# Kernel tuning notes

Measured on AMD Instinct MI355X. Metric: run time of the kernel, lower is better.

## Reference

```python
import jax, jax.numpy as jnp
import numpy as np

B = 65536
IN_DIM = 512
H0, H1 = 256, 128
HEAD_H = 64
D = 12
K_MAX = 3
EPS = 1e-5
# predecessor indices per disease (topologically ordered DAG)
PRED_LISTS = [[], [0], [0], [1, 2], [0, 3], [2], [4, 5], [1, 6], [3, 7], [6, 8], [5, 9], [8, 10, 9]]


def setup_inputs() -> dict:
    key = jax.random.key(0)
    ks = jax.random.split(key, 16)
    x = jax.random.normal(ks[0], (B, IN_DIM), jnp.float32)
    enc_W0 = jax.random.normal(ks[1], (IN_DIM, H0), jnp.float32) * 0.04
    enc_b0 = jnp.zeros((H0,), jnp.float32)
    bn0_g = jnp.ones((H0,), jnp.float32)
    bn0_b = jnp.zeros((H0,), jnp.float32)
    bn0_m = jax.random.normal(ks[2], (H0,), jnp.float32) * 0.1
    bn0_v = jax.random.uniform(ks[3], (H0,), jnp.float32, 0.5, 1.5)
    enc_W1 = jax.random.normal(ks[4], (H0, H1), jnp.float32) * 0.06
    enc_b1 = jnp.zeros((H1,), jnp.float32)
    bn1_g = jnp.ones((H1,), jnp.float32)
    bn1_b = jnp.zeros((H1,), jnp.float32)
    bn1_m = jax.random.normal(ks[5], (H1,), jnp.float32) * 0.1
    bn1_v = jax.random.uniform(ks[6], (H1,), jnp.float32, 0.5, 1.5)
    w_init = jax.random.normal(ks[7], (D, H1), jnp.float32) * 0.09   # head.layer1 (pass-1 logit)
    b_init = jnp.zeros((D,), jnp.float32)
    Wz = jax.random.normal(ks[8], (D, H1, HEAD_H), jnp.float32) * 0.09   # head first layer, z-columns
    Wp = jax.random.normal(ks[9], (D, K_MAX, HEAD_H), jnp.float32) * 0.09  # head first layer, predecessor columns (padded)
    bh = jnp.zeros((D, HEAD_H), jnp.float32)
    Wo = jax.random.normal(ks[10], (D, HEAD_H), jnp.float32) * 0.12
    bo = jnp.zeros((D,), jnp.float32)
    idx = np.zeros((D, K_MAX), np.int32)
    w = np.zeros((D, K_MAX), np.float32)
    for d, preds in enumerate(PRED_LISTS):
        for j, p in enumerate(preds):
            idx[d, j] = p
            w[d, j] = 0.5  # DAG edge weight; zero entries are padding
    return {"x": x, "enc_W0": enc_W0, "enc_b0": enc_b0, "bn0_g": bn0_g, "bn0_b": bn0_b,
            "bn0_m": bn0_m, "bn0_v": bn0_v, "enc_W1": enc_W1, "enc_b1": enc_b1,
            "bn1_g": bn1_g, "bn1_b": bn1_b, "bn1_m": bn1_m, "bn1_v": bn1_v,
            "w_init": w_init, "b_init": b_init, "Wz": Wz, "Wp": Wp, "bh": bh,
            "Wo": Wo, "bo": bo, "pred_w": jnp.asarray(w), "pred_idx": jnp.asarray(idx)}


def reference(x, enc_W0, enc_b0, bn0_g, bn0_b, bn0_m, bn0_v, enc_W1, enc_b1,
              bn1_g, bn1_b, bn1_m, bn1_v, w_init, b_init, Wz, Wp, bh, Wo, bo,
              pred_w, pred_idx):
    # Shared encoder: Linear -> BatchNorm(eval stats) -> ReLU, twice (dropout identity at eval)
    h = x @ enc_W0 + enc_b0
    h = jax.nn.relu((h - bn0_m) * jax.lax.rsqrt(bn0_v + EPS) * bn0_g + bn0_b)
    z = h @ enc_W1 + enc_b1
    z = jax.nn.relu((z - bn1_m) * jax.lax.rsqrt(bn1_v + EPS) * bn1_g + bn1_b)  # [B, H1]
    # Pass 1: initial per-disease prediction = sigmoid(head.layer1(z))
    p = jax.nn.sigmoid(z @ w_init.T + b_init)  # [B, D]
    # Pass 2: DAG gather of predecessor predictions, edge-weighted; padding slots have weight 0
    aug = p[:, pred_idx] * pred_w  # [B, D, K_MAX]
    # Per-disease head: Linear(H1 + k -> HEAD_H) split into z-part + predecessor-part, ReLU, Linear(HEAD_H -> 1), sigmoid
    hid = jax.nn.relu(jnp.einsum('be,deh->bdh', z, Wz) + jnp.einsum('bdk,dkh->bdh', aug, Wp) + bh)
    out = jax.nn.sigmoid(jnp.einsum('bdh,dh->bd', hid, Wo) + bo)  # [B, D] = torch.cat of final_preds
    return out
```

## Files before the change

kernel.cpp:

```cpp
#include <hip/hip_runtime.h>
#include <stdint.h>

#define B_TOT   65536
#define IN_DIM  512
#define H0      256
#define H1      128
#define HH      64
#define NDIS    12

typedef __bf16 bf16_t;
typedef __bf16 bf16x4 __attribute__((ext_vector_type(4)));
typedef __bf16 bf16x8 __attribute__((ext_vector_type(8)));
typedef float  f32x4  __attribute__((ext_vector_type(4)));

#define WS_W0T   0u
#define WS_W1T   262144u
#define WS_WZT   327680u
#define WS_WIT   524288u
#define WS_AL0   528384u
#define WS_BE0   529408u
#define WS_AL1   530432u
#define WS_BE1   530944u
#define WS_NEED  531456u

#define L_PS     17408u
#define L_PART   22528u
#define L_TOTAL  34816u

__device__ __forceinline__ f32x4 MF(bf16x8 a, bf16x8 b, f32x4 c) {
    return __builtin_amdgcn_mfma_f32_16x16x32_bf16(a, b, c, 0, 0, 0);
}
__device__ __forceinline__ void BAR() {
    asm volatile("s_waitcnt lgkmcnt(0)\n\ts_barrier" ::: "memory");
}

#define PACK8(o, lo, hi) { o[0]=(bf16_t)lo[0]; o[1]=(bf16_t)lo[1]; o[2]=(bf16_t)lo[2]; o[3]=(bf16_t)lo[3]; \
                           o[4]=(bf16_t)hi[0]; o[5]=(bf16_t)hi[1]; o[6]=(bf16_t)hi[2]; o[7]=(bf16_t)hi[3]; }

__global__ void prep_kernel(const float* __restrict__ W0, const float* __restrict__ b0,
                            const float* __restrict__ g0, const float* __restrict__ bb0,
                            const float* __restrict__ mm0, const float* __restrict__ vv0,
                            const float* __restrict__ W1, const float* __restrict__ b1,
                            const float* __restrict__ g1, const float* __restrict__ bb1,
                            const float* __restrict__ mm1, const float* __restrict__ vv1,
                            const float* __restrict__ w_init, const float* __restrict__ Wz,
                            char* __restrict__ ws)
{
    bf16_t* W0t = (bf16_t*)(ws + WS_W0T);
    bf16_t* W1t = (bf16_t*)(ws + WS_W1T);
    bf16_t* Wzt = (bf16_t*)(ws + WS_WZT);
    bf16_t* wiT = (bf16_t*)(ws + WS_WIT);
    float* al0 = (float*)(ws + WS_AL0);
    float* be0 = (float*)(ws + WS_BE0);
    float* al1 = (float*)(ws + WS_AL1);
    float* be1 = (float*)(ws + WS_BE1);

    int t = blockIdx.x * 256 + threadIdx.x;

    {
        int c = t >> 9, k = t & 511;
        W0t[t] = (bf16_t)W0[k * H0 + c];
    }
    if (t < H1 * H0) {
        int c = t >> 8, k = t & 255;
        W1t[t] = (bf16_t)W1[k * H1 + c];
    }
    if (t < NDIS * HH * H1) {
        int d = t >> 13, r = t & 8191, h = r >> 7, e = r & 127;
        Wzt[t] = (bf16_t)Wz[d * 8192 + e * 64 + h];
    }
    if (t < 16 * H1) {
        int d = t >> 7, e = t & 127;
        wiT[t] = (d < NDIS) ? (bf16_t)w_init[d * H1 + e] : (bf16_t)0.0f;
    }
    if (t < H0) {
        float a = g0[t] * rsqrtf(vv0[t] + 1e-5f);
        al0[t] = a;
        be0[t] = (b0[t] - mm0[t]) * a + bb0[t];
    }
    if (t < H1) {
        float a = g1[t] * rsqrtf(vv1[t] + 1e-5f);
        al1[t] = a;
        be1[t] = (b1[t] - mm1[t]) * a + bb1[t];
    }
}

__global__ __launch_bounds__(256, 4) void fused_kernel(
    const float* __restrict__ x,
    const bf16_t* __restrict__ W0t, const bf16_t* __restrict__ W1t,
    const float* __restrict__ al0, const float* __restrict__ be0,
    const float* __restrict__ al1, const float* __restrict__ be1,
    const bf16_t* __restrict__ Wzt, const bf16_t* __restrict__ wiT,
    const float* __restrict__ b_init, const float* __restrict__ Wp,
    const float* __restrict__ bh, const float* __restrict__ Wo,
    const float* __restrict__ bo, const float* __restrict__ pred_w,
    const int* __restrict__ pred_idx, float* __restrict__ out)
{
    __shared__ __align__(16) char smem[L_TOTAL];

    const int tid  = threadIdx.x;
    const int lane = tid & 63, wid = tid >> 6;
    const int l15 = lane & 15, lg = lane >> 4;
    const int m0 = blockIdx.x * 64;

    bf16_t* xs = (bf16_t*)smem;

    const float *sgp0, *sgp1;
    int sd0, sd1;
    {
        int f0 = tid, f1 = tid + 256;
        int r0 = f0 >> 3, s0 = f0 & 7, r1 = f1 >> 3, s1 = f1 & 7;
        sgp0 = x + (size_t)(m0 + r0) * IN_DIM + s0 * 8;
        sgp1 = x + (size_t)(m0 + r1) * IN_DIM + s1 * 8;
        sd0 = r0 * 64 + ((s0 ^ (r0 & 7)) << 3);
        sd1 = r1 * 64 + ((s1 ^ (r1 & 7)) << 3);
    }
    const bf16_t* wg = W0t + (size_t)(wid * 64 + l15) * IN_DIM + lg * 8;
    const int xb0 = ((lg ^ (l15 & 7)) << 3);
    const int xb1 = (((4 | lg) ^ (l15 & 7)) << 3);
    const int xrow = l15 * 64;

    f32x4 acc[4][4] = {};
    f32x4 lo0, hi0, lo1, hi1;

    lo0 = *(const f32x4*)(sgp0);     hi0 = *(const f32x4*)(sgp0 + 4);
    lo1 = *(const f32x4*)(sgp1);     hi1 = *(const f32x4*)(sgp1 + 4);
    { bf16x8 o; PACK8(o, lo0, hi0); *(bf16x8*)(xs + sd0) = o; }
    { bf16x8 o; PACK8(o, lo1, hi1); *(bf16x8*)(xs + sd1) = o; }
    lo0 = *(const f32x4*)(sgp0 + 64); hi0 = *(const f32x4*)(sgp0 + 68);
    lo1 = *(const f32x4*)(sgp1 + 64); hi1 = *(const f32x4*)(sgp1 + 68);
    BAR();

    #pragma unroll 1
    for (int ks = 0; ks < 8; ++ks) {
        bf16x8 a0[4], a1[4];
        #pragma unroll
        for (int mf = 0; mf < 4; ++mf) {
            a0[mf] = *(const bf16x8*)(wg + mf * 16 * IN_DIM + ks * 64);
            a1[mf] = *(const bf16x8*)(wg + mf * 16 * IN_DIM + ks * 64 + 32);
        }
        if (ks < 7) {
            bf16_t* xw = xs + ((ks + 1) & 1) * 4096;
            { bf16x8 o; PACK8(o, lo0, hi0); *(bf16x8*)(xw + sd0) = o; }
            { bf16x8 o; PACK8(o, lo1, hi1); *(bf16x8*)(xw + sd1) = o; }
            if (ks < 6) {
                lo0 = *(const f32x4*)(sgp0 + (ks + 2) * 64); hi0 = *(const f32x4*)(sgp0 + (ks + 2) * 64 + 4);
                lo1 = *(const f32x4*)(sgp1 + (ks + 2) * 64); hi1 = *(const f32x4*)(sgp1 + (ks + 2) * 64 + 4);
            }
        }
        const bf16_t* xr = xs + (ks & 1) * 4096;
        #pragma unroll
        for (int nf = 0; nf < 4; ++nf) {
            bf16x8 b = *(const bf16x8*)(xr + nf * 1024 + xrow + xb0);
            #pragma unroll
            for (int mf = 0; mf < 4; ++mf) acc[mf][nf] = MF(a0[mf], b, acc[mf][nf]);
        }
        #pragma unroll
        for (int nf = 0; nf < 4; ++nf) {
            bf16x8 b = *(const bf16x8*)(xr + nf * 1024 + xrow + xb1);
            #pragma unroll
            for (int mf = 0; mf < 4; ++mf) acc[mf][nf] = MF(a1[mf], b, acc[mf][nf]);
        }
        BAR();
    }

    {
        bf16_t* hs = (bf16_t*)smem;
        #pragma unroll
        for (int mf = 0; mf < 4; ++mf) {
            int c = wid * 64 + mf * 16 + lg * 4;
            f32x4 al = *(const f32x4*)(al0 + c);
            f32x4 be = *(const f32x4*)(be0 + c);
            #pragma unroll
            for (int nf = 0; nf < 4; ++nf) {
                int r = nf * 16 + l15;
                bf16x4 o;
                #pragma unroll
                for (int j = 0; j < 4; ++j)
                    o[j] = (bf16_t)fmaxf(acc[mf][nf][j] * al[j] + be[j], 0.f);
                *(bf16x4*)(hs + r * 264 + c) = o;
            }
        }
    }
    BAR();

    f32x4 acc2[2][4] = {};
    {
        const bf16_t* hs  = (const bf16_t*)smem;
        const bf16_t* w1g = W1t + (size_t)(wid * 32 + l15) * H0 + lg * 8;
        bf16x8 aP[2], aQ[2];
        aP[0] = *(const bf16x8*)(w1g);
        aP[1] = *(const bf16x8*)(w1g + 16 * H0);
        aQ[0] = *(const bf16x8*)(w1g + 32);
        aQ[1] = *(const bf16x8*)(w1g + 16 * H0 + 32);
        #pragma unroll
        for (int kf = 0; kf < 8; ++kf) {
            bf16x8 ac0 = (kf & 1) ? aQ[0] : aP[0];
            bf16x8 ac1 = (kf & 1) ? aQ[1] : aP[1];
            if (kf < 6) {
                if (kf & 1) {
                    aQ[0] = *(const bf16x8*)(w1g + (kf + 2) * 32);
                    aQ[1] = *(const bf16x8*)(w1g + 16 * H0 + (kf + 2) * 32);
                } else {
                    aP[0] = *(const bf16x8*)(w1g + (kf + 2) * 32);
                    aP[1] = *(const bf16x8*)(w1g + 16 * H0 + (kf + 2) * 32);
                }
            }
            #pragma unroll
            for (int nf = 0; nf < 4; ++nf) {
                bf16x8 b = *(const bf16x8*)(hs + (nf * 16 + l15) * 264 + kf * 32 + lg * 8);
                acc2[0][nf] = MF(ac0, b, acc2[0][nf]);
                acc2[1][nf] = MF(ac1, b, acc2[1][nf]);
            }
        }
    }
    BAR();
    {
        bf16_t* zs = (bf16_t*)smem;
        #pragma unroll
        for (int mf = 0; mf < 2; ++mf) {
            int c = wid * 32 + mf * 16 + lg * 4;
            f32x4 al = *(const f32x4*)(al1 + c);
            f32x4 be = *(const f32x4*)(be1 + c);
            #pragma unroll
            for (int nf = 0; nf < 4; ++nf) {
                int r = nf * 16 + l15;
                bf16x4 o;
                #pragma unroll
                for (int j = 0; j < 4; ++j)
                    o[j] = (bf16_t)fmaxf(acc2[mf][nf][j] * al[j] + be[j], 0.f);
                *(bf16x4*)(zs + r * 136 + c) = o;
            }
        }
    }
    BAR();

    const bf16_t* zs = (const bf16_t*)smem;
    float* psf  = (float*)(smem + L_PS);
    float* part = (float*)(smem + L_PART);
    const bf16_t* wzg = Wzt + (size_t)(wid * 16 + l15) * H1 + lg * 8;

    bf16x8 az0 = *(const bf16x8*)(wzg);
    bf16x8 az1 = *(const bf16x8*)(wzg + 32);
    bf16x8 az2 = *(const bf16x8*)(wzg + 64);
    bf16x8 az3 = *(const bf16x8*)(wzg + 96);

    {
        f32x4 pacc = {};
        #pragma unroll
        for (int kf = 0; kf < 4; ++kf) {
            bf16x8 aw = *(const bf16x8*)(wiT + l15 * H1 + kf * 32 + lg * 8);
            bf16x8 bz = *(const bf16x8*)(zs + (wid * 16 + l15) * 136 + kf * 32 + lg * 8);
            pacc = MF(aw, bz, pacc);
        }
        f32x4 pv;
        #pragma unroll
        for (int j = 0; j < 4; ++j) {
            int d = lg * 4 + j;
            float bi = (d < NDIS) ? b_init[d] : 0.f;
            pv[j] = 1.f / (1.f + __expf(-(pacc[j] + bi)));
        }
        *(f32x4*)(psf + (wid * 16 + l15) * 20 + lg * 4) = pv;
    }
    BAR();

    #pragma unroll 1
    for (int d = 0; d < NDIS; ++d) {
        bf16x8 an0 = az0, an1 = az1, an2 = az2, an3 = az3;
        if (d < NDIS - 1) {
            const bf16_t* p = wzg + (size_t)(d + 1) * 8192;
            an0 = *(const bf16x8*)(p);      an1 = *(const bf16x8*)(p + 32);
            an2 = *(const bf16x8*)(p + 64); an3 = *(const bf16x8*)(p + 96);
        }
        int i0 = pred_idx[d * 3 + 0], i1 = pred_idx[d * 3 + 1], i2 = pred_idx[d * 3 + 2];
        float wq0 = pred_w[d * 3 + 0], wq1 = pred_w[d * 3 + 1], wq2 = pred_w[d * 3 + 2];
        int hb = wid * 16 + lg * 4;
        f32x4 bhv = *(const f32x4*)(bh + d * 64 + hb);
        f32x4 wov = *(const f32x4*)(Wo + d * 64 + hb);
        f32x4 wpa = *(const f32x4*)(Wp + d * 192 + hb);
        f32x4 wpb = *(const f32x4*)(Wp + d * 192 + 64 + hb);
        f32x4 wpc = *(const f32x4*)(Wp + d * 192 + 128 + hb);

        #pragma unroll
        for (int nf = 0; nf < 4; ++nf) {
            const bf16_t* zr = zs + (nf * 16 + l15) * 136 + lg * 8;
            f32x4 hacc = {};
            hacc = MF(az0, *(const bf16x8*)(zr),      hacc);
            hacc = MF(az1, *(const bf16x8*)(zr + 32), hacc);
            hacc = MF(az2, *(const bf16x8*)(zr + 64), hacc);
            hacc = MF(az3, *(const bf16x8*)(zr + 96), hacc);
            int r = nf * 16 + l15;
            float a0 = psf[r * 20 + i0] * wq0;
            float a1 = psf[r * 20 + i1] * wq1;
            float a2 = psf[r * 20 + i2] * wq2;
            float s = 0.f;
            #pragma unroll
            for (int j = 0; j < 4; ++j) {
                float v = hacc[j] + bhv[j] + a0 * wpa[j] + a1 * wpb[j] + a2 * wpc[j];
                s += fmaxf(v, 0.f) * wov[j];
            }
            s += __shfl_xor(s, 16);
            s += __shfl_xor(s, 32);
            if (lane < 16) part[d * 256 + r * 4 + wid] = s;
        }
        az0 = an0; az1 = an1; az2 = an2; az3 = an3;
    }
    BAR();

    {
        float* obuf = (float*)(smem + L_PS);
        #pragma unroll
        for (int i = 0; i < 3; ++i) {
            int e = tid * 3 + i;
            int d = e % 12, r = e / 12;
            f32x4 p = *(const f32x4*)(part + d * 256 + r * 4);
            float s = p[0] + p[1] + p[2] + p[3] + bo[d];
            obuf[e] = 1.f / (1.f + __expf(-s));
        }
    }
    BAR();
    if (tid < 192) {
        f32x4 o = *(const f32x4*)((const float*)(smem + L_PS) + tid * 4);
        *(f32x4*)(out + (size_t)blockIdx.x * 768 + tid * 4) = o;
    }
}

extern "C" void kernel_launch(void* const* d_in, const int* in_sizes, int n_in,
                              void* d_out, int out_size, void* d_ws, size_t ws_size,
                              hipStream_t stream) {
    if (ws_size < (size_t)WS_NEED) return;

    const float* x      = (const float*)d_in[0];
    const float* W0     = (const float*)d_in[1];
    const float* b0     = (const float*)d_in[2];
    const float* g0     = (const float*)d_in[3];
    const float* bb0    = (const float*)d_in[4];
    const float* mm0    = (const float*)d_in[5];
    const float* vv0    = (const float*)d_in[6];
    const float* W1     = (const float*)d_in[7];
    const float* b1     = (const float*)d_in[8];
    const float* g1     = (const float*)d_in[9];
    const float* bb1    = (const float*)d_in[10];
    const float* mm1    = (const float*)d_in[11];
    const float* vv1    = (const float*)d_in[12];
    const float* w_init = (const float*)d_in[13];
    const float* b_init = (const float*)d_in[14];
    const float* Wz     = (const float*)d_in[15];
    const float* Wp     = (const float*)d_in[16];
    const float* bh     = (const float*)d_in[17];
    const float* Wo     = (const float*)d_in[18];
    const float* bo     = (const float*)d_in[19];
    const float* pred_w = (const float*)d_in[20];
    const int*   pred_idx = (const int*)d_in[21];

    char* ws = (char*)d_ws;
    const bf16_t* W0t = (const bf16_t*)(ws + WS_W0T);
    const bf16_t* W1t = (const bf16_t*)(ws + WS_W1T);
    const bf16_t* Wzt = (const bf16_t*)(ws + WS_WZT);
    const bf16_t* wiT = (const bf16_t*)(ws + WS_WIT);
    const float* al0 = (const float*)(ws + WS_AL0);
    const float* be0 = (const float*)(ws + WS_BE0);
    const float* al1 = (const float*)(ws + WS_AL1);
    const float* be1 = (const float*)(ws + WS_BE1);

    prep_kernel<<<dim3(512), dim3(256), 0, stream>>>(
        W0, b0, g0, bb0, mm0, vv0, W1, b1, g1, bb1, mm1, vv1, w_init, Wz, ws);

    fused_kernel<<<dim3(B_TOT / 64), dim3(256), 0, stream>>>(
        x, W0t, W1t, al0, be0, al1, be1, Wzt, wiT, b_init, Wp, bh, Wo, bo,
        pred_w, pred_idx, (float*)d_out);
}
```

Before: 94.30 us.

## Halve row tile to 32 rows with two waves per block

Each block now handles 32 batch rows with 128 threads (two waves) instead of 64 rows with four waves, so each wave covers twice as many output columns in every GEMM stage. The head stage keeps the z fragments in registers and computes two hidden-unit groups per wave, and the cross-wave reduction buffer shrinks to two partials. The aim is more blocks and smaller LDS for better occupancy and load balance. In exchange, W0/W1/Wz weights are re-read from global/L2 twice as often per row, the software prefetch of the next disease's Wz fragments is gone, and register pressure rises from larger accumulator arrays.

```diff
diff --git a/kernel.cpp b/kernel.cpp
--- a/kernel.cpp
+++ b/kernel.cpp
@@ -7,6 +7,9 @@
 #define H1      128
 #define HH      64
 #define NDIS    12
+
+#define BM      32
+#define NBLK    (B_TOT / BM)
 
 typedef __bf16 bf16_t;
 typedef __bf16 bf16x4 __attribute__((ext_vector_type(4)));
@@ -23,9 +26,9 @@
 #define WS_BE1   530944u
 #define WS_NEED  531456u
 
-#define L_PS     17408u
-#define L_PART   22528u
-#define L_TOTAL  34816u
+#define L_PS     8704u
+#define L_PART   11264u
+#define L_TOTAL  17408u
 
 __device__ __forceinline__ f32x4 MF(bf16x8 a, bf16x8 b, f32x4 c) {
     return __builtin_amdgcn_mfma_f32_16x16x32_bf16(a, b, c, 0, 0, 0);
@@ -85,7 +88,7 @@
     }
 }
 
-__global__ __launch_bounds__(256, 4) void fused_kernel(
+__global__ __launch_bounds__(128, 4) void fused_kernel(
     const float* __restrict__ x,
     const bf16_t* __restrict__ W0t, const bf16_t* __restrict__ W1t,
     const float* __restrict__ al0, const float* __restrict__ be0,
@@ -99,28 +102,27 @@
     __shared__ __align__(16) char smem[L_TOTAL];
 
     const int tid  = threadIdx.x;
-    const int lane = tid & 63, wid = tid >> 6;
+    const int lane = tid & 63, w = tid >> 6;
     const int l15 = lane & 15, lg = lane >> 4;
-    const int m0 = blockIdx.x * 64;
+    const int m0 = blockIdx.x * BM;
 
     bf16_t* xs = (bf16_t*)smem;
 
     const float *sgp0, *sgp1;
     int sd0, sd1;
     {
-        int f0 = tid, f1 = tid + 256;
+        int f0 = tid, f1 = tid + 128;
         int r0 = f0 >> 3, s0 = f0 & 7, r1 = f1 >> 3, s1 = f1 & 7;
         sgp0 = x + (size_t)(m0 + r0) * IN_DIM + s0 * 8;
         sgp1 = x + (size_t)(m0 + r1) * IN_DIM + s1 * 8;
         sd0 = r0 * 64 + ((s0 ^ (r0 & 7)) << 3);
         sd1 = r1 * 64 + ((s1 ^ (r1 & 7)) << 3);
     }
-    const bf16_t* wg = W0t + (size_t)(wid * 64 + l15) * IN_DIM + lg * 8;
+    const bf16_t* wg = W0t + (size_t)(w * 128 + l15) * IN_DIM + lg * 8;
     const int xb0 = ((lg ^ (l15 & 7)) << 3);
     const int xb1 = (((4 | lg) ^ (l15 & 7)) << 3);
-    const int xrow = l15 * 64;
-
-    f32x4 acc[4][4] = {};
+
+    f32x4 acc[8][2] = {};
     f32x4 lo0, hi0, lo1, hi1;
 
     lo0 = *(const f32x4*)(sgp0);     hi0 = *(const f32x4*)(sgp0 + 4);
@@ -133,14 +135,8 @@
 
     #pragma unroll 1
     for (int ks = 0; ks < 8; ++ks) {
-        bf16x8 a0[4], a1[4];
-        #pragma unroll
-        for (int mf = 0; mf < 4; ++mf) {
-            a0[mf] = *(const bf16x8*)(wg + mf * 16 * IN_DIM + ks * 64);
-            a1[mf] = *(const bf16x8*)(wg + mf * 16 * IN_DIM + ks * 64 + 32);
-        }
         if (ks < 7) {
-            bf16_t* xw = xs + ((ks + 1) & 1) * 4096;
+            bf16_t* xw = xs + ((ks + 1) & 1) * 2048;
             { bf16x8 o; PACK8(o, lo0, hi0); *(bf16x8*)(xw + sd0) = o; }
             { bf16x8 o; PACK8(o, lo1, hi1); *(bf16x8*)(xw + sd1) = o; }
             if (ks < 6) {
@@ -148,18 +144,30 @@
                 lo1 = *(const f32x4*)(sgp1 + (ks + 2) * 64); hi1 = *(const f32x4*)(sgp1 + (ks + 2) * 64 + 4);
             }
         }
-        const bf16_t* xr = xs + (ks & 1) * 4096;
-        #pragma unroll
-        for (int nf = 0; nf < 4; ++nf) {
-            bf16x8 b = *(const bf16x8*)(xr + nf * 1024 + xrow + xb0);
-            #pragma unroll
-            for (int mf = 0; mf < 4; ++mf) acc[mf][nf] = MF(a0[mf], b, acc[mf][nf]);
-        }
-        #pragma unroll
-        for (int nf = 0; nf < 4; ++nf) {
-            bf16x8 b = *(const bf16x8*)(xr + nf * 1024 + xrow + xb1);
-            #pragma unroll
-            for (int mf = 0; mf < 4; ++mf) acc[mf][nf] = MF(a1[mf], b, acc[mf][nf]);
+        const bf16_t* xr = xs + (ks & 1) * 2048;
+        {
+            bf16x8 a[8];
+            #pragma unroll
+            for (int mf = 0; mf < 8; ++mf)
+                a[mf] = *(const bf16x8*)(wg + (size_t)mf * 16 * IN_DIM + ks * 64);
+            #pragma unroll
+            for (int nf = 0; nf < 2; ++nf) {
+                bf16x8 b = *(const bf16x8*)(xr + (nf * 16 + l15) * 64 + xb0);
+                #pragma unroll
+                for (int mf = 0; mf < 8; ++mf) acc[mf][nf] = MF(a[mf], b, acc[mf][nf]);
+            }
+        }
+        {
+            bf16x8 a[8];
+            #pragma unroll
+            for (int mf = 0; mf < 8; ++mf)
+                a[mf] = *(const bf16x8*)(wg + (size_t)mf * 16 * IN_DIM + ks * 64 + 32);
+            #pragma unroll
+            for (int nf = 0; nf < 2; ++nf) {
+                bf16x8 b = *(const bf16x8*)(xr + (nf * 16 + l15) * 64 + xb1);
+                #pragma unroll
+                for (int mf = 0; mf < 8; ++mf) acc[mf][nf] = MF(a[mf], b, acc[mf][nf]);
+            }
         }
         BAR();
     }
@@ -167,12 +175,12 @@
     {
         bf16_t* hs = (bf16_t*)smem;
         #pragma unroll
-        for (int mf = 0; mf < 4; ++mf) {
-            int c = wid * 64 + mf * 16 + lg * 4;
+        for (int mf = 0; mf < 8; ++mf) {
+            int c = w * 128 + mf * 16 + lg * 4;
             f32x4 al = *(const f32x4*)(al0 + c);
             f32x4 be = *(const f32x4*)(be0 + c);
             #pragma unroll
-            for (int nf = 0; nf < 4; ++nf) {
+            for (int nf = 0; nf < 2; ++nf) {
                 int r = nf * 16 + l15;
                 bf16x4 o;
                 #pragma unroll
@@ -184,33 +192,32 @@
     }
     BAR();
 
-    f32x4 acc2[2][4] = {};
+    f32x4 acc2[4][2] = {};
     {
         const bf16_t* hs  = (const bf16_t*)smem;
-        const bf16_t* w1g = W1t + (size_t)(wid * 32 + l15) * H0 + lg * 8;
-        bf16x8 aP[2], aQ[2];
-        aP[0] = *(const bf16x8*)(w1g);
-        aP[1] = *(const bf16x8*)(w1g + 16 * H0);
-        aQ[0] = *(const bf16x8*)(w1g + 32);
-        aQ[1] = *(const bf16x8*)(w1g + 16 * H0 + 32);
+        const bf16_t* w1g = W1t + (size_t)(w * 64 + l15) * H0 + lg * 8;
+        bf16x8 aP[4], aQ[4];
+        #pragma unroll
+        for (int mf = 0; mf < 4; ++mf) aP[mf] = *(const bf16x8*)(w1g + (size_t)mf * 16 * H0);
+        #pragma unroll
+        for (int mf = 0; mf < 4; ++mf) aQ[mf] = *(const bf16x8*)(w1g + (size_t)mf * 16 * H0 + 32);
         #pragma unroll
         for (int kf = 0; kf < 8; ++kf) {
-            bf16x8 ac0 = (kf & 1) ? aQ[0] : aP[0];
-            bf16x8 ac1 = (kf & 1) ? aQ[1] : aP[1];
+            bf16x8 ac[4];
+            #pragma unroll
+            for (int mf = 0; mf < 4; ++mf) ac[mf] = (kf & 1) ? aQ[mf] : aP[mf];
             if (kf < 6) {
-                if (kf & 1) {
-                    aQ[0] = *(const bf16x8*)(w1g + (kf + 2) * 32);
-                    aQ[1] = *(const bf16x8*)(w1g + 16 * H0 + (kf + 2) * 32);
-                } else {
-                    aP[0] = *(const bf16x8*)(w1g + (kf + 2) * 32);
-                    aP[1] = *(const bf16x8*)(w1g + 16 * H0 + (kf + 2) * 32);
+                #pragma unroll
+                for (int mf = 0; mf < 4; ++mf) {
+                    bf16x8 nv = *(const bf16x8*)(w1g + (size_t)mf * 16 * H0 + (kf + 2) * 32);
+                    if (kf & 1) aQ[mf] = nv; else aP[mf] = nv;
                 }
             }
             #pragma unroll
-            for (int nf = 0; nf < 4; ++nf) {
+            for (int nf = 0; nf < 2; ++nf) {
                 bf16x8 b = *(const bf16x8*)(hs + (nf * 16 + l15) * 264 + kf * 32 + lg * 8);
-                acc2[0][nf] = MF(ac0, b, acc2[0][nf]);
-                acc2[1][nf] = MF(ac1, b, acc2[1][nf]);
+                #pragma unroll
+                for (int mf = 0; mf < 4; ++mf) acc2[mf][nf] = MF(ac[mf], b, acc2[mf][nf]);
             }
         }
     }
@@ -218,12 +225,12 @@
     {
         bf16_t* zs = (bf16_t*)smem;
         #pragma unroll
-        for (int mf = 0; mf < 2; ++mf) {
-            int c = wid * 32 + mf * 16 + lg * 4;
+        for (int mf = 0; mf < 4; ++mf) {
+            int c = w * 64 + mf * 16 + lg * 4;
             f32x4 al = *(const f32x4*)(al1 + c);
             f32x4 be = *(const f32x4*)(be1 + c);
             #pragma unroll
-            for (int nf = 0; nf < 4; ++nf) {
+            for (int nf = 0; nf < 2; ++nf) {
                 int r = nf * 16 + l15;
                 bf16x4 o;
                 #pragma unroll
@@ -238,19 +245,13 @@
     const bf16_t* zs = (const bf16_t*)smem;
     float* psf  = (float*)(smem + L_PS);
     float* part = (float*)(smem + L_PART);
-    const bf16_t* wzg = Wzt + (size_t)(wid * 16 + l15) * H1 + lg * 8;
-
-    bf16x8 az0 = *(const bf16x8*)(wzg);
-    bf16x8 az1 = *(const bf16x8*)(wzg + 32);
-    bf16x8 az2 = *(const bf16x8*)(wzg + 64);
-    bf16x8 az3 = *(const bf16x8*)(wzg + 96);
 
     {
         f32x4 pacc = {};
         #pragma unroll
         for (int kf = 0; kf < 4; ++kf) {
             bf16x8 aw = *(const bf16x8*)(wiT + l15 * H1 + kf * 32 + lg * 8);
-            bf16x8 bz = *(const bf16x8*)(zs + (wid * 16 + l15) * 136 + kf * 32 + lg * 8);
+            bf16x8 bz = *(const bf16x8*)(zs + (w * 16 + l15) * 136 + kf * 32 + lg * 8);
             pacc = MF(aw, bz, pacc);
         }
         f32x4 pv;
@@ -260,50 +261,66 @@
             float bi = (d < NDIS) ? b_init[d] : 0.f;
             pv[j] = 1.f / (1.f + __expf(-(pacc[j] + bi)));
         }
-        *(f32x4*)(psf + (wid * 16 + l15) * 20 + lg * 4) = pv;
-    }
-    BAR();
+        *(f32x4*)(psf + (w * 16 + l15) * 20 + lg * 4) = pv;
+    }
+    BAR();
+
+    bf16x8 zb[2][4];
+    #pragma unroll
+    for (int nf = 0; nf < 2; ++nf)
+        #pragma unroll
+        for (int kf = 0; kf < 4; ++kf)
+            zb[nf][kf] = *(const bf16x8*)(zs + (nf * 16 + l15) * 136 + kf * 32 + lg * 8);
+
+    const bf16_t* wzg = Wzt + (size_t)(w * 32 + l15) * H1 + lg * 8;
 
     #pragma unroll 1
     for (int d = 0; d < NDIS; ++d) {
-        bf16x8 an0 = az0, an1 = az1, an2 = az2, an3 = az3;
-        if (d < NDIS - 1) {
-            const bf16_t* p = wzg + (size_t)(d + 1) * 8192;
-            an0 = *(const bf16x8*)(p);      an1 = *(const bf16x8*)(p + 32);
-            an2 = *(const bf16x8*)(p + 64); an3 = *(const bf16x8*)(p + 96);
-        }
+        const bf16_t* wd = wzg + (size_t)d * 8192;
+        bf16x8 az[2][4];
+        #pragma unroll
+        for (int hg = 0; hg < 2; ++hg)
+            #pragma unroll
+            for (int eg = 0; eg < 4; ++eg)
+                az[hg][eg] = *(const bf16x8*)(wd + (size_t)hg * 16 * H1 + eg * 32);
+
+        f32x4 hacc[2][2] = {};
+        #pragma unroll
+        for (int hg = 0; hg < 2; ++hg)
+            #pragma unroll
+            for (int eg = 0; eg < 4; ++eg)
+                #pragma unroll
+                for (int nf = 0; nf < 2; ++nf)
+                    hacc[hg][nf] = MF(az[hg][eg], zb[nf][eg], hacc[hg][nf]);
+
         int i0 = pred_idx[d * 3 + 0], i1 = pred_idx[d * 3 + 1], i2 = pred_idx[d * 3 + 2];
         float wq0 = pred_w[d * 3 + 0], wq1 = pred_w[d * 3 + 1], wq2 = pred_w[d * 3 + 2];
-        int hb = wid * 16 + lg * 4;
-        f32x4 bhv = *(const f32x4*)(bh + d * 64 + hb);
-        f32x4 wov = *(const f32x4*)(Wo + d * 64 + hb);
-        f32x4 wpa = *(const f32x4*)(Wp + d * 192 + hb);
-        f32x4 wpb = *(const f32x4*)(Wp + d * 192 + 64 + hb);
-        f32x4 wpc = *(const f32x4*)(Wp + d * 192 + 128 + hb);
-
-        #pragma unroll
-        for (int nf = 0; nf < 4; ++nf) {
-            const bf16_t* zr = zs + (nf * 16 + l15) * 136 + lg * 8;
-            f32x4 hacc = {};
-            hacc = MF(az0, *(const bf16x8*)(zr),      hacc);
-            hacc = MF(az1, *(const bf16x8*)(zr + 32), hacc);
-            hacc = MF(az2, *(const bf16x8*)(zr + 64), hacc);
-            hacc = MF(az3, *(const bf16x8*)(zr + 96), hacc);
+
+        #pragma unroll
+        for (int nf = 0; nf < 2; ++nf) {
             int r = nf * 16 + l15;
             float a0 = psf[r * 20 + i0] * wq0;
             float a1 = psf[r * 20 + i1] * wq1;
             float a2 = psf[r * 20 + i2] * wq2;
             float s = 0.f;
             #pragma unroll
-            for (int j = 0; j < 4; ++j) {
-                float v = hacc[j] + bhv[j] + a0 * wpa[j] + a1 * wpb[j] + a2 * wpc[j];
-                s += fmaxf(v, 0.f) * wov[j];
+            for (int hg = 0; hg < 2; ++hg) {
+                int hb = w * 32 + hg * 16 + lg * 4;
+                f32x4 bhv = *(const f32x4*)(bh + d * 64 + hb);
+                f32x4 wov = *(const f32x4*)(Wo + d * 64 + hb);
+                f32x4 wpa = *(const f32x4*)(Wp + d * 192 + hb);
+                f32x4 wpb = *(const f32x4*)(Wp + d * 192 + 64 + hb);
+                f32x4 wpc = *(const f32x4*)(Wp + d * 192 + 128 + hb);
+                #pragma unroll
+                for (int j = 0; j < 4; ++j) {
+                    float v = hacc[hg][nf][j] + bhv[j] + a0 * wpa[j] + a1 * wpb[j] + a2 * wpc[j];
+                    s += fmaxf(v, 0.f) * wov[j];
+                }
             }
             s += __shfl_xor(s, 16);
             s += __shfl_xor(s, 32);
-            if (lane < 16) part[d * 256 + r * 4 + wid] = s;
-        }
-        az0 = an0; az1 = an1; az2 = an2; az3 = an3;
+            if (lane < 16) part[d * 64 + r * 2 + w] = s;
+        }
     }
     BAR();
 
@@ -313,15 +330,14 @@
         for (int i = 0; i < 3; ++i) {
             int e = tid * 3 + i;
             int d = e % 12, r = e / 12;
-            f32x4 p = *(const f32x4*)(part + d * 256 + r * 4);
-            float s = p[0] + p[1] + p[2] + p[3] + bo[d];
+            float s = part[d * 64 + r * 2] + part[d * 64 + r * 2 + 1] + bo[d];
             obuf[e] = 1.f / (1.f + __expf(-s));
         }
     }
     BAR();
-    if (tid < 192) {
+    if (tid < 96) {
         f32x4 o = *(const f32x4*)((const float*)(smem + L_PS) + tid * 4);
-        *(f32x4*)(out + (size_t)blockIdx.x * 768 + tid * 4) = o;
+        *(f32x4*)(out + (size_t)blockIdx.x * 384 + tid * 4) = o;
     }
 }
 
@@ -366,7 +382,7 @@
     prep_kernel<<<dim3(512), dim3(256), 0, stream>>>(
         W0, b0, g0, bb0, mm0, vv0, W1, b1, g1, bb1, mm1, vv1, w_init, Wz, ws);
 
-    fused_kernel<<<dim3(B_TOT / 64), dim3(256), 0, stream>>>(
+    fused_kernel<<<dim3(NBLK), dim3(128), 0, stream>>>(
         x, W0t, W1t, al0, be0, al1, be1, Wzt, wiT, b_init, Wp, bh, Wo, bo,
         pred_w, pred_idx, (float*)d_out);
 }
```

Measured after the change: 180.0 us. +90.8%, slower.

## Stream x tiles via direct global-to-LDS loads with triple buffering

Applied to the files above, without the earlier changes.

Replaces the register-staged fp32-to-bf16 x loading with global_load_lds DMA of raw fp32 tiles into a triple-buffered, XOR-swizzled LDS ring. Weight fragments are double-buffered, and the bf16 conversion moves to LDS read time. The head loop now prefetches the next disease's small parameters. This aims to overlap the memory-bound x stream with MFMA work and to remove VGPR staging. In exchange it uses more LDS (49KB) and lowers the occupancy target from 4 to 3 blocks per CU.

```diff
diff --git a/kernel.cpp b/kernel.cpp
--- a/kernel.cpp
+++ b/kernel.cpp
@@ -7,6 +7,9 @@
 #define H1      128
 #define HH      64
 #define NDIS    12
+
+#define BM      64
+#define NBLK    (B_TOT / BM)
 
 typedef __bf16 bf16_t;
 typedef __bf16 bf16x4 __attribute__((ext_vector_type(4)));
@@ -25,14 +28,20 @@
 
 #define L_PS     17408u
 #define L_PART   22528u
-#define L_TOTAL  34816u
+#define L_TOTAL  49152u
 
 __device__ __forceinline__ f32x4 MF(bf16x8 a, bf16x8 b, f32x4 c) {
     return __builtin_amdgcn_mfma_f32_16x16x32_bf16(a, b, c, 0, 0, 0);
 }
+__device__ __forceinline__ void dma16(const void* g, void* l) {
+    __builtin_amdgcn_global_load_lds(
+        (const __attribute__((address_space(1))) unsigned*)g,
+        (__attribute__((address_space(3))) unsigned*)l, 16, 0, 0);
+}
 __device__ __forceinline__ void BAR() {
-    asm volatile("s_waitcnt lgkmcnt(0)\n\ts_barrier" ::: "memory");
-}
+    asm volatile("s_waitcnt lgkmcnt(0)\ns_barrier" ::: "memory");
+}
+#define WAITBAR(N) asm volatile("s_waitcnt vmcnt(" #N ") lgkmcnt(0)\ns_barrier" ::: "memory")
 
 #define PACK8(o, lo, hi) { o[0]=(bf16_t)lo[0]; o[1]=(bf16_t)lo[1]; o[2]=(bf16_t)lo[2]; o[3]=(bf16_t)lo[3]; \
                            o[4]=(bf16_t)hi[0]; o[5]=(bf16_t)hi[1]; o[6]=(bf16_t)hi[2]; o[7]=(bf16_t)hi[3]; }
@@ -85,7 +94,7 @@
     }
 }
 
-__global__ __launch_bounds__(256, 4) void fused_kernel(
+__global__ __launch_bounds__(256, 3) void fused_kernel(
     const float* __restrict__ x,
     const bf16_t* __restrict__ W0t, const bf16_t* __restrict__ W1t,
     const float* __restrict__ al0, const float* __restrict__ be0,
@@ -99,76 +108,67 @@
     __shared__ __align__(16) char smem[L_TOTAL];
 
     const int tid  = threadIdx.x;
-    const int lane = tid & 63, wid = tid >> 6;
+    const int lane = tid & 63, w = tid >> 6;
     const int l15 = lane & 15, lg = lane >> 4;
-    const int m0 = blockIdx.x * 64;
-
-    bf16_t* xs = (bf16_t*)smem;
-
-    const float *sgp0, *sgp1;
-    int sd0, sd1;
-    {
-        int f0 = tid, f1 = tid + 256;
-        int r0 = f0 >> 3, s0 = f0 & 7, r1 = f1 >> 3, s1 = f1 & 7;
-        sgp0 = x + (size_t)(m0 + r0) * IN_DIM + s0 * 8;
-        sgp1 = x + (size_t)(m0 + r1) * IN_DIM + s1 * 8;
-        sd0 = r0 * 64 + ((s0 ^ (r0 & 7)) << 3);
-        sd1 = r1 * 64 + ((s1 ^ (r1 & 7)) << 3);
-    }
-    const bf16_t* wg = W0t + (size_t)(wid * 64 + l15) * IN_DIM + lg * 8;
-    const int xb0 = ((lg ^ (l15 & 7)) << 3);
-    const int xb1 = (((4 | lg) ^ (l15 & 7)) << 3);
-    const int xrow = l15 * 64;
+    const int m0 = blockIdx.x * BM;
+
+    const float* xsrc[4];
+    float* xdst[4];
+    #pragma unroll
+    for (int i = 0; i < 4; ++i) {
+        int row = w * 16 + i * 4 + (lane >> 4);
+        int gslot = (lane & 15) ^ (row & 15);
+        xsrc[i] = x + (size_t)(m0 + row) * IN_DIM + gslot * 4;
+        xdst[i] = (float*)smem + (w * 16 + i * 4) * 64;
+    }
+    const bf16_t* wg = W0t + (size_t)(w * 64 + l15) * IN_DIM + lg * 8;
 
     f32x4 acc[4][4] = {};
-    f32x4 lo0, hi0, lo1, hi1;
-
-    lo0 = *(const f32x4*)(sgp0);     hi0 = *(const f32x4*)(sgp0 + 4);
-    lo1 = *(const f32x4*)(sgp1);     hi1 = *(const f32x4*)(sgp1 + 4);
-    { bf16x8 o; PACK8(o, lo0, hi0); *(bf16x8*)(xs + sd0) = o; }
-    { bf16x8 o; PACK8(o, lo1, hi1); *(bf16x8*)(xs + sd1) = o; }
-    lo0 = *(const f32x4*)(sgp0 + 64); hi0 = *(const f32x4*)(sgp0 + 68);
-    lo1 = *(const f32x4*)(sgp1 + 64); hi1 = *(const f32x4*)(sgp1 + 68);
-    BAR();
-
-    #pragma unroll 1
-    for (int ks = 0; ks < 8; ++ks) {
-        bf16x8 a0[4], a1[4];
+    bf16x8 aA[2][4], aB[2][4];
+
+#define ISSUE_DMA(K) { _Pragma("unroll") \
+    for (int i = 0; i < 4; ++i) dma16(xsrc[i] + (K) * 64, xdst[i] + ((K) % 3) * 4096); }
+#define ISSUE_A(K, SET) { _Pragma("unroll") \
+    for (int mf = 0; mf < 4; ++mf) { \
+        SET[0][mf] = *(const bf16x8*)(wg + (size_t)mf * 16 * IN_DIM + (K) * 64); \
+        SET[1][mf] = *(const bf16x8*)(wg + (size_t)mf * 16 * IN_DIM + (K) * 64 + 32); } }
+#define MFMA_STEP(K, CUR) { \
+    const float* xb = (const float*)smem + ((K) % 3) * 1024 * 4; \
+    __builtin_amdgcn_s_setprio(1); \
+    _Pragma("unroll") \
+    for (int kf = 0; kf < 2; ++kf) { \
+        _Pragma("unroll") \
+        for (int nf = 0; nf < 4; ++nf) { \
+            int s0 = kf * 8 + lg * 2; \
+            f32x4 u = *(const f32x4*)(xb + (nf * 16 + l15) * 64 + ((s0    ) ^ l15) * 4); \
+            f32x4 v = *(const f32x4*)(xb + (nf * 16 + l15) * 64 + ((s0 + 1) ^ l15) * 4); \
+            bf16x8 b; PACK8(b, u, v); \
+            _Pragma("unroll") \
+            for (int mf = 0; mf < 4; ++mf) acc[mf][nf] = MF(CUR[kf][mf], b, acc[mf][nf]); \
+        } \
+    } \
+    __builtin_amdgcn_s_setprio(0); }
+
+    ISSUE_DMA(0);
+    ISSUE_A(0, aA);
+    ISSUE_DMA(1);
+
+    WAITBAR(12); ISSUE_DMA(2); ISSUE_A(1, aB); MFMA_STEP(0, aA);
+    WAITBAR(12); ISSUE_DMA(3); ISSUE_A(2, aA); MFMA_STEP(1, aB);
+    WAITBAR(12); ISSUE_DMA(4); ISSUE_A(3, aB); MFMA_STEP(2, aA);
+    WAITBAR(12); ISSUE_DMA(5); ISSUE_A(4, aA); MFMA_STEP(3, aB);
+    WAITBAR(12); ISSUE_DMA(6); ISSUE_A(5, aB); MFMA_STEP(4, aA);
+    WAITBAR(12); ISSUE_DMA(7); ISSUE_A(6, aA); MFMA_STEP(5, aB);
+    WAITBAR(12);               ISSUE_A(7, aB); MFMA_STEP(6, aA);
+    WAITBAR(8);                                MFMA_STEP(7, aB);
+
+    asm volatile("s_waitcnt vmcnt(0) lgkmcnt(0)\ns_barrier" ::: "memory");
+
+    {
+        bf16_t* hs = (bf16_t*)smem;
         #pragma unroll
         for (int mf = 0; mf < 4; ++mf) {
-            a0[mf] = *(const bf16x8*)(wg + mf * 16 * IN_DIM + ks * 64);
-            a1[mf] = *(const bf16x8*)(wg + mf * 16 * IN_DIM + ks * 64 + 32);
-        }
-        if (ks < 7) {
-            bf16_t* xw = xs + ((ks + 1) & 1) * 4096;
-            { bf16x8 o; PACK8(o, lo0, hi0); *(bf16x8*)(xw + sd0) = o; }
-            { bf16x8 o; PACK8(o, lo1, hi1); *(bf16x8*)(xw + sd1) = o; }
-            if (ks < 6) {
-                lo0 = *(const f32x4*)(sgp0 + (ks + 2) * 64); hi0 = *(const f32x4*)(sgp0 + (ks + 2) * 64 + 4);
-                lo1 = *(const f32x4*)(sgp1 + (ks + 2) * 64); hi1 = *(const f32x4*)(sgp1 + (ks + 2) * 64 + 4);
-            }
-        }
-        const bf16_t* xr = xs + (ks & 1) * 4096;
-        #pragma unroll
-        for (int nf = 0; nf < 4; ++nf) {
-            bf16x8 b = *(const bf16x8*)(xr + nf * 1024 + xrow + xb0);
-            #pragma unroll
-            for (int mf = 0; mf < 4; ++mf) acc[mf][nf] = MF(a0[mf], b, acc[mf][nf]);
-        }
-        #pragma unroll
-        for (int nf = 0; nf < 4; ++nf) {
-            bf16x8 b = *(const bf16x8*)(xr + nf * 1024 + xrow + xb1);
-            #pragma unroll
-            for (int mf = 0; mf < 4; ++mf) acc[mf][nf] = MF(a1[mf], b, acc[mf][nf]);
-        }
-        BAR();
-    }
-
-    {
-        bf16_t* hs = (bf16_t*)smem;
-        #pragma unroll
-        for (int mf = 0; mf < 4; ++mf) {
-            int c = wid * 64 + mf * 16 + lg * 4;
+            int c = w * 64 + mf * 16 + lg * 4;
             f32x4 al = *(const f32x4*)(al0 + c);
             f32x4 be = *(const f32x4*)(be0 + c);
             #pragma unroll
@@ -187,7 +187,7 @@
     f32x4 acc2[2][4] = {};
     {
         const bf16_t* hs  = (const bf16_t*)smem;
-        const bf16_t* w1g = W1t + (size_t)(wid * 32 + l15) * H0 + lg * 8;
+        const bf16_t* w1g = W1t + (size_t)(w * 32 + l15) * H0 + lg * 8;
         bf16x8 aP[2], aQ[2];
         aP[0] = *(const bf16x8*)(w1g);
         aP[1] = *(const bf16x8*)(w1g + 16 * H0);
@@ -219,7 +219,7 @@
         bf16_t* zs = (bf16_t*)smem;
         #pragma unroll
         for (int mf = 0; mf < 2; ++mf) {
-            int c = wid * 32 + mf * 16 + lg * 4;
+            int c = w * 32 + mf * 16 + lg * 4;
             f32x4 al = *(const f32x4*)(al1 + c);
             f32x4 be = *(const f32x4*)(be1 + c);
             #pragma unroll
@@ -238,19 +238,27 @@
     const bf16_t* zs = (const bf16_t*)smem;
     float* psf  = (float*)(smem + L_PS);
     float* part = (float*)(smem + L_PART);
-    const bf16_t* wzg = Wzt + (size_t)(wid * 16 + l15) * H1 + lg * 8;
+    const bf16_t* wzg = Wzt + (size_t)(w * 16 + l15) * H1 + lg * 8;
+    const int hb = w * 16 + lg * 4;
 
     bf16x8 az0 = *(const bf16x8*)(wzg);
     bf16x8 az1 = *(const bf16x8*)(wzg + 32);
     bf16x8 az2 = *(const bf16x8*)(wzg + 64);
     bf16x8 az3 = *(const bf16x8*)(wzg + 96);
+    int   ci0 = pred_idx[0], ci1 = pred_idx[1], ci2 = pred_idx[2];
+    float cq0 = pred_w[0],  cq1 = pred_w[1],  cq2 = pred_w[2];
+    f32x4 cbh = *(const f32x4*)(bh + hb);
+    f32x4 cwo = *(const f32x4*)(Wo + hb);
+    f32x4 cpa = *(const f32x4*)(Wp + hb);
+    f32x4 cpb = *(const f32x4*)(Wp + 64 + hb);
+    f32x4 cpc = *(const f32x4*)(Wp + 128 + hb);
 
     {
         f32x4 pacc = {};
         #pragma unroll
         for (int kf = 0; kf < 4; ++kf) {
             bf16x8 aw = *(const bf16x8*)(wiT + l15 * H1 + kf * 32 + lg * 8);
-            bf16x8 bz = *(const bf16x8*)(zs + (wid * 16 + l15) * 136 + kf * 32 + lg * 8);
+            bf16x8 bz = *(const bf16x8*)(zs + (w * 16 + l15) * 136 + kf * 32 + lg * 8);
             pacc = MF(aw, bz, pacc);
         }
         f32x4 pv;
@@ -260,26 +268,28 @@
             float bi = (d < NDIS) ? b_init[d] : 0.f;
             pv[j] = 1.f / (1.f + __expf(-(pacc[j] + bi)));
         }
-        *(f32x4*)(psf + (wid * 16 + l15) * 20 + lg * 4) = pv;
+        *(f32x4*)(psf + (w * 16 + l15) * 20 + lg * 4) = pv;
     }
     BAR();
 
     #pragma unroll 1
     for (int d = 0; d < NDIS; ++d) {
         bf16x8 an0 = az0, an1 = az1, an2 = az2, an3 = az3;
+        int   ni0 = ci0, ni1 = ci1, ni2 = ci2;
+        float nq0 = cq0, nq1 = cq1, nq2 = cq2;
+        f32x4 nbh = cbh, nwo = cwo, npa = cpa, npb = cpb, npc = cpc;
         if (d < NDIS - 1) {
             const bf16_t* p = wzg + (size_t)(d + 1) * 8192;
             an0 = *(const bf16x8*)(p);      an1 = *(const bf16x8*)(p + 32);
             an2 = *(const bf16x8*)(p + 64); an3 = *(const bf16x8*)(p + 96);
-        }
-        int i0 = pred_idx[d * 3 + 0], i1 = pred_idx[d * 3 + 1], i2 = pred_idx[d * 3 + 2];
-        float wq0 = pred_w[d * 3 + 0], wq1 = pred_w[d * 3 + 1], wq2 = pred_w[d * 3 + 2];
-        int hb = wid * 16 + lg * 4;
-        f32x4 bhv = *(const f32x4*)(bh + d * 64 + hb);
-        f32x4 wov = *(const f32x4*)(Wo + d * 64 + hb);
-        f32x4 wpa = *(const f32x4*)(Wp + d * 192 + hb);
-        f32x4 wpb = *(const f32x4*)(Wp + d * 192 + 64 + hb);
-        f32x4 wpc = *(const f32x4*)(Wp + d * 192 + 128 + hb);
+            ni0 = pred_idx[(d + 1) * 3]; ni1 = pred_idx[(d + 1) * 3 + 1]; ni2 = pred_idx[(d + 1) * 3 + 2];
+            nq0 = pred_w[(d + 1) * 3];   nq1 = pred_w[(d + 1) * 3 + 1];   nq2 = pred_w[(d + 1) * 3 + 2];
+            nbh = *(const f32x4*)(bh + (d + 1) * 64 + hb);
+            nwo = *(const f32x4*)(Wo + (d + 1) * 64 + hb);
+            npa = *(const f32x4*)(Wp + (d + 1) * 192 + hb);
+            npb = *(const f32x4*)(Wp + (d + 1) * 192 + 64 + hb);
+            npc = *(const f32x4*)(Wp + (d + 1) * 192 + 128 + hb);
+        }
 
         #pragma unroll
         for (int nf = 0; nf < 4; ++nf) {
@@ -290,20 +300,23 @@
             hacc = MF(az2, *(const bf16x8*)(zr + 64), hacc);
             hacc = MF(az3, *(const bf16x8*)(zr + 96), hacc);
             int r = nf * 16 + l15;
-            float a0 = psf[r * 20 + i0] * wq0;
-            float a1 = psf[r * 20 + i1] * wq1;
-            float a2 = psf[r * 20 + i2] * wq2;
+            float a0 = psf[r * 20 + ci0] * cq0;
+            float a1 = psf[r * 20 + ci1] * cq1;
+            float a2 = psf[r * 20 + ci2] * cq2;
             float s = 0.f;
             #pragma unroll
             for (int j = 0; j < 4; ++j) {
-                float v = hacc[j] + bhv[j] + a0 * wpa[j] + a1 * wpb[j] + a2 * wpc[j];
-                s += fmaxf(v, 0.f) * wov[j];
+                float v = hacc[j] + cbh[j] + a0 * cpa[j] + a1 * cpb[j] + a2 * cpc[j];
+                s += fmaxf(v, 0.f) * cwo[j];
             }
             s += __shfl_xor(s, 16);
             s += __shfl_xor(s, 32);
-            if (lane < 16) part[d * 256 + r * 4 + wid] = s;
+            if (lane < 16) part[d * 256 + r * 4 + w] = s;
         }
         az0 = an0; az1 = an1; az2 = an2; az3 = an3;
+        ci0 = ni0; ci1 = ni1; ci2 = ni2;
+        cq0 = nq0; cq1 = nq1; cq2 = nq2;
+        cbh = nbh; cwo = nwo; cpa = npa; cpb = npb; cpc = npc;
     }
     BAR();
 
@@ -366,7 +379,7 @@
     prep_kernel<<<dim3(512), dim3(256), 0, stream>>>(
         W0, b0, g0, bb0, mm0, vv0, W1, b1, g1, bb1, mm1, vv1, w_init, Wz, ws);
 
-    fused_kernel<<<dim3(B_TOT / 64), dim3(256), 0, stream>>>(
+    fused_kernel<<<dim3(NBLK), dim3(256), 0, stream>>>(
         x, W0t, W1t, al0, be0, al1, be1, Wzt, wiT, b_init, Wp, bh, Wo, bo,
         pred_w, pred_idx, (float*)d_out);
 }
```

Measured after the change: 95.94 us. About the same (+1.7%).
